# Performance work log

Measured on AMD Instinct MI355X. Metric: run time of the kernel, lower is better.

## Reference

```python
import jax, jax.numpy as jnp
import numpy as np

INP = 1024          # inp_size
N = 8000            # n_neurons
NE = 6400           # n_e_neurons = 0.8*N
NI = 1600           # n_i_neurons = 0.2*N
TS = 1000           # ts_sim = t_sim/dt = 1.0/0.001
PRB0, PRB1 = 200, 1000  # probe window in timesteps
DT = 0.001
TAU = 0.02
VTH = 0.5
RATE = 0.5          # rate_scale
NORM = float(PRB1 - PRB0)  # spike_p_norm


def setup_inputs() -> dict:
    key = jax.random.key(0)
    k1, k2, k3, k4, k5, k6 = jax.random.split(key, 6)
    inp = jax.random.uniform(k1, (INP,), dtype=jnp.float32)
    A = INP + N
    # Sparse random recurrent weights, faithful in structure to init_w:
    # rows [0:INP+NE] carry excitatory (positive) weights, last NI rows inhibitory (negative).
    sign = jnp.concatenate([jnp.ones(INP + NE, jnp.float32), -jnp.ones(NI, jnp.float32)])[:, None]
    mask_e = (jax.random.uniform(k2, (A, NE)) < 0.05).astype(jnp.float32)
    w_ae = sign * mask_e * jax.random.uniform(k3, (A, NE), dtype=jnp.float32) * 0.1
    mask_i = (jax.random.uniform(k4, (A, NI)) < 0.05).astype(jnp.float32)
    w_ai = sign * mask_i * jax.random.uniform(k5, (A, NI), dtype=jnp.float32) * 0.1
    # Precomputed per-timestep uniform noise (replaces torch.rand_like in the loop)
    rand_p = jax.random.uniform(k6, (TS, INP), dtype=jnp.float32)
    return {"inp": inp, "w_ae": w_ae, "w_ai": w_ai, "rand_p": rand_p}


def reference(inp, w_ae, w_ai, rand_p):
    inp_s = inp * RATE
    decay = 1.0 - DT / TAU  # vmem += -vmem/tau*dt  ==  vmem *= (1 - dt/tau)

    def step(carry, r):
        vmem, sl, slp = carry  # spike_l, spike_l_prev as float32 {0,1}
        sp = (r <= inp_s).astype(jnp.float32)  # Poisson input spikes
        v = vmem * decay
        # excitatory targets see prev-step E spikes + current I spikes; inhibitory the reverse
        in_e = jnp.concatenate([sp, slp[:NE], sl[NE:]])   # [INP+N]
        in_i = jnp.concatenate([sp, sl[:NE], slp[NE:]])   # [INP+N]
        v = v + jnp.concatenate([in_e @ w_ae, in_i @ w_ai])  # [N]
        new_sl = (v >= VTH).astype(jnp.float32)
        v = v * (1.0 - new_sl)  # reset fired neurons to 0
        return (v, new_sl, sl), new_sl[:NE]

    init = (jnp.zeros(N, jnp.float32), jnp.zeros(N, jnp.float32), jnp.zeros(N, jnp.float32))
    _, e_spikes = jax.lax.scan(step, init, rand_p)  # [TS, NE]
    sumspike_e = e_spikes[PRB0:PRB1].sum(axis=0)
    return sumspike_e / NORM
```

## Files before the change

### kernel.cpp

```cpp
#include <hip/hip_runtime.h>
#include <stdint.h>

#define INP_N   1024
#define NE_N    6400
#define NI_N    1600
#define NCOL    8000
#define TS_N    1000
#define PRB0_T  200
#define TSPLIT  16
#define NCHUNK  12
#define CAPTOT  992
#define IN_ENT  112
#define BC      64
#define CAPQ    36
#define CAPMAX  88

enum : size_t {
  ROWS_OFF = 0,
  VALS_OFF = ROWS_OFF + (size_t)CAPTOT * NCOL * 2,
  CNT_OFF  = VALS_OFF + (size_t)CAPTOT * NCOL * 4,
  CSUM_OFF = CNT_OFF  + (size_t)NCHUNK * NCOL * 4,
  INPM_OFF = CSUM_OFF + (size_t)NCHUNK * NCOL * 4,
  DRV_OFF  = INPM_OFF + (size_t)TS_N * 16 * 8,
  SE_OFF   = DRV_OFF  + (size_t)TS_N * NCOL * 4,
  SI_OFF   = SE_OFF   + (size_t)NCOL * 4,
  FLG_OFF  = SI_OFF   + (size_t)NCOL * 4,
  STV_OFF  = FLG_OFF  + (size_t)TS_N * 4,
  STR_OFF  = STV_OFF  + (size_t)8192 * 4,
  STT_OFF  = STR_OFF  + (size_t)512 * 8,
  SAB_OFF  = STT_OFF  + (size_t)8 * 4,
  AFL_OFF  = SAB_OFF  + 4,
  MNP_OFF  = AFL_OFF  + 4,
  MNW_OFF  = MNP_OFF  + 32 * 4,
  OVF_OFF  = MNW_OFF  + 64 * 4,
  STG_OFF  = OVF_OFF  + 4,
};

__device__ __forceinline__ void chunk_info(int c, int& j0, int& len, int& cap, int& off) {
  if (c < 2) { j0 = c * 512;            len = 512; cap = 56; off = c * 56; }
  else       { j0 = 1024 + (c - 2) * 800; len = 800; cap = 88; off = 112 + (c - 2) * 88; }
}

__global__ void k_spikes(const float* __restrict__ rand_p,
                         const float* __restrict__ inp,
                         unsigned long long* __restrict__ inpmask,
                         float* __restrict__ gv, unsigned long long* __restrict__ gring,
                         int* __restrict__ gtot, int* __restrict__ ovf) {
  int gid = blockIdx.x * blockDim.x + threadIdx.x;
  if (gid < 8192) gv[gid] = 0.f;
  if (gid < 512)  gring[gid] = 0ull;
  if (gid < 8)    gtot[gid] = 0;
  if (gid == 0)   ovf[0] = 0;
  int i = gid & (INP_N - 1);
  int pred = rand_p[gid] <= inp[i] * 0.5f;
  unsigned long long b = __ballot(pred != 0);
  if ((threadIdx.x & 63) == 0) inpmask[gid >> 6] = b;
}

__global__ void __launch_bounds__(256) k_build(
    const float* __restrict__ w_ae, const float* __restrict__ w_ai,
    uint16_t* __restrict__ rows, float* __restrict__ vals,
    int* __restrict__ cnt, float* __restrict__ csum, int* __restrict__ ovf) {
  __shared__ uint16_t rs_s[4 * CAPQ * BC];
  __shared__ float    vs_s[4 * CAPQ * BC];
  __shared__ int      kqs[4][BC];
  __shared__ float    sqs[4][BC];
  const int tid   = threadIdx.x;
  const int lane  = tid & 63;
  const int wv    = tid >> 6;
  const int chunk = blockIdx.y;
  const int col0  = blockIdx.x * BC;
  int j0, len, cap, off;
  chunk_info(chunk, j0, len, cap, off);
  const float* W; int nc, cc0;
  if (col0 < NE_N) { W = w_ae; nc = NE_N; cc0 = col0; }
  else             { W = w_ai; nc = NI_N; cc0 = col0 - NE_N; }

  const int qlen = len >> 2;
  const int j0w  = j0 + wv * qlen;
  const float* Wc = W + (size_t)j0w * nc + cc0 + lane;

  float cur[16], nxt[16];
  #pragma unroll
  for (int r = 0; r < 16; ++r)
    cur[r] = Wc[(size_t)r * nc];

  int k = 0; float s = 0.f; int ovfl = 0;
  for (int t0 = 0; t0 < qlen; t0 += 16) {
    const int nt = t0 + 16;
    if (nt < qlen) {
      #pragma unroll
      for (int r = 0; r < 16; ++r) {
        int rq = nt + r; rq = rq < qlen ? rq : qlen - 1;
        nxt[r] = Wc[(size_t)rq * nc];
      }
    }
    const int rlim = (qlen - t0) < 16 ? (qlen - t0) : 16;
    #pragma unroll
    for (int r = 0; r < 16; ++r) {
      if (r < rlim) {
        float w = cur[r];
        if (w != 0.f) {
          if (k < CAPQ) {
            rs_s[(wv * CAPQ + k) * BC + lane] = (uint16_t)(j0w + t0 + r);
            vs_s[(wv * CAPQ + k) * BC + lane] = w;
            s += w; ++k;
          } else ovfl = 1;
        }
      }
    }
    #pragma unroll
    for (int r = 0; r < 16; ++r) cur[r] = nxt[r];
  }
  kqs[wv][lane] = k;
  sqs[wv][lane] = s;
  if (ovfl) atomicOr(ovf, 1);
  __syncthreads();

  const int col = lane;
  const int k0 = kqs[0][col], k1 = kqs[1][col], k2 = kqs[2][col], k3 = kqs[3][col];
  const int c1 = k0, c2 = k0 + k1, c3 = c2 + k2, ktot = c3 + k3;
  if (tid < BC) {
    cnt[chunk * NCOL + col0 + col]  = ktot < cap ? ktot : cap;
    csum[chunk * NCOL + col0 + col] = ((sqs[0][col] + sqs[1][col]) + sqs[2][col]) + sqs[3][col];
    if (ktot > cap) atomicOr(ovf, 1);
  }
  const size_t gb = (size_t)off * NCOL + col0;
  for (int kk = wv; kk < cap; kk += 4) {
    uint16_t rr = (uint16_t)j0; float vv = 0.f;
    if (kk < ktot) {
      int q, loc;
      if      (kk < c1) { q = 0; loc = kk; }
      else if (kk < c2) { q = 1; loc = kk - c1; }
      else if (kk < c3) { q = 2; loc = kk - c2; }
      else              { q = 3; loc = kk - c3; }
      rr = rs_s[(q * CAPQ + loc) * BC + col];
      vv = vs_s[(q * CAPQ + loc) * BC + col];
    }
    rows[gb + (size_t)kk * NCOL + col] = rr;
    vals[gb + (size_t)kk * NCOL + col] = vv;
  }
}

__global__ void __launch_bounds__(256) k_proof(
    const float* __restrict__ csum, float* __restrict__ sE, float* __restrict__ sI,
    const float* __restrict__ vals, float* __restrict__ minpart, float* __restrict__ mwpart) {
  const int tid = threadIdx.x;
  const int b = blockIdx.x;
  float m = 1e30f;
  if (b < 32) {
    int col = b * 256 + tid;
    if (col < NCOL) {
      float se = 0.f;
      #pragma unroll
      for (int c = 2; c <= 9; ++c) se += csum[c * NCOL + col];
      float si = csum[10 * NCOL + col] + csum[11 * NCOL + col];
      sE[col] = se;
      sI[col] = si;
      m = se + si;
    }
  } else {
    const int n = IN_ENT * NCOL;
    for (int i = (b - 32) * 256 + tid; i < n; i += 64 * 256)
      m = fminf(m, vals[i]);
  }
  #pragma unroll
  for (int o = 32; o; o >>= 1) m = fminf(m, __shfl_down(m, o));
  __shared__ float w4[4];
  if ((tid & 63) == 0) w4[tid >> 6] = m;
  __syncthreads();
  if (tid == 0) {
    float r = fminf(fminf(w4[0], w4[1]), fminf(w4[2], w4[3]));
    if (b < 32) minpart[b] = r; else mwpart[b - 32] = r;
  }
}

__global__ void k_strong(const float* __restrict__ minpart, const float* __restrict__ mwpart,
                         const int* __restrict__ ovf, int* __restrict__ strongp) {
  int t = threadIdx.x;
  float mb = (t < 32) ? minpart[t] : 1e30f;
  float mw = mwpart[t];
  #pragma unroll
  for (int o = 32; o; o >>= 1) {
    mb = fminf(mb, __shfl_down(mb, o));
    mw = fminf(mw, __shfl_down(mw, o));
  }
  if (t == 0)
    strongp[0] = (mb >= 1.0f && mw >= 0.0f && ovf[0] == 0) ? 1 : 0;
}

__global__ void __launch_bounds__(256) k_drive(
    const uint16_t* __restrict__ rows, const float* __restrict__ vals,
    const unsigned long long* __restrict__ inpmask, float* __restrict__ drive,
    const int* __restrict__ strongp, const int* __restrict__ sabp, int pass) {
  int t0, t1;
  if (pass == 0) {
    if (strongp[0]) {
      if (blockIdx.y >= 4) return;
      t0 = blockIdx.y * 4; t1 = t0 + 4;
    } else { t0 = blockIdx.y * 40; t1 = t0 + 40; }
  } else {
    if (!strongp[0] || sabp[0]) return;
    t0 = blockIdx.y * 40; t1 = t0 + 40;
    if (blockIdx.y == 0) t0 = TSPLIT;
  }
  __shared__ uint16_t rs[IN_ENT * 64];
  __shared__ float    vs[IN_ENT * 64];
  __shared__ float    act0[INP_N];
  __shared__ float    psum[4][64];
  const int tid = threadIdx.x, lane = tid & 63, ph = tid >> 6;
  const int col0 = blockIdx.x * 64;
  for (int idx = tid; idx < IN_ENT * 64; idx += 256) {
    int k = idx >> 6, l = idx & 63;
    rs[idx] = rows[(size_t)k * NCOL + col0 + l];
    vs[idx] = vals[(size_t)k * NCOL + col0 + l];
  }
  __syncthreads();
  for (int t = t0; t < t1; ++t) {
    #pragma unroll
    for (int i = tid; i < INP_N; i += 256)
      act0[i] = (float)((inpmask[(size_t)t * 16 + (i >> 6)] >> (i & 63)) & 1ull);
    __syncthreads();
    float acc = 0.f;
    for (int k = ph; k < IN_ENT; k += 4)
      acc += vs[k * 64 + lane] * act0[rs[k * 64 + lane]];
    psum[ph][lane] = acc;
    __syncthreads();
    if (ph == 0)
      drive[(size_t)t * NCOL + col0 + lane] =
        ((psum[0][lane] + psum[1][lane]) + psum[2][lane]) + psum[3][lane];
    __syncthreads();
  }
}

__global__ void __launch_bounds__(512) k_step(
    const uint16_t* __restrict__ rows, const float* __restrict__ vals,
    const int* __restrict__ cnt, const float* __restrict__ sE,
    const float* __restrict__ sI, const float* __restrict__ drive,
    float* __restrict__ gv, unsigned long long* __restrict__ gring,
    int* __restrict__ gtot, const int* __restrict__ strongp, int t) {
  __shared__ unsigned long long m[128];
  __shared__ float psum[8][64];
  const int tid = threadIdx.x, lane = tid & 63, ph = tid >> 6;
  const int blk = blockIdx.x;
  const bool isE = (blk < 100);
  const int sw = t & 3, s1 = (t + 3) & 3, s2 = (t + 2) & 3;

  const bool full1 = (gtot[s1] == NE_N) && (gtot[4 + s1] == NI_N);
  const bool full2 = (gtot[s2] == NE_N) && (gtot[4 + s2] == NI_N);
  if (strongp[0] && full1 && full2) {
    if (tid == 0) {
      gring[sw * 128 + blk] = ~0ull;
      if (blk == 0) { gtot[sw] = NE_N; gtot[4 + sw] = NI_N; }
    }
    return;
  }

  const int sEs = isE ? s2 : s1;
  const int sIs = isE ? s1 : s2;
  const int col = blk * 64 + lane;

  if (tid < 100)      m[tid] = gring[sEs * 128 + tid];
  else if (tid < 125) m[tid] = gring[sIs * 128 + tid];
  const int pEv = gtot[sEs];
  const int pIv = gtot[4 + sIs];
  if (blk == 0 && tid == 0) { gtot[(t + 1) & 3] = 0; gtot[4 + ((t + 1) & 3)] = 0; }
  __syncthreads();

  float acc = 0.f;
  if (pEv > 0 && pEv < NE_N) {
    for (int c = 2; c <= 9; ++c) {
      int cn = cnt[c * NCOL + col];
      size_t base = (size_t)(112 + (c - 2) * 88) * NCOL + col;
      for (int k = ph; k < cn; k += 8) {
        int r = rows[base + (size_t)k * NCOL] - 1024;
        float wv = vals[base + (size_t)k * NCOL];
        if ((m[r >> 6] >> (r & 63)) & 1ull) acc += wv;
      }
    }
  }
  if (pIv > 0 && pIv < NI_N) {
    for (int c = 10; c <= 11; ++c) {
      int cn = cnt[c * NCOL + col];
      size_t base = (size_t)(112 + (c - 2) * 88) * NCOL + col;
      for (int k = ph; k < cn; k += 8) {
        int r = rows[base + (size_t)k * NCOL] - 1024;
        float wv = vals[base + (size_t)k * NCOL];
        if ((m[r >> 6] >> (r & 63)) & 1ull) acc += wv;
      }
    }
  }
  psum[ph][lane] = acc;
  __syncthreads();

  if (ph == 0) {
    float tot = drive[(size_t)t * NCOL + col]
              + ((psum[0][lane] + psum[1][lane]) + (psum[2][lane] + psum[3][lane]))
              + ((psum[4][lane] + psum[5][lane]) + (psum[6][lane] + psum[7][lane]));
    if (pEv == NE_N) tot += sE[col];
    if (pIv == NI_N) tot += sI[col];
    float vn = gv[col] * 0.95f + tot;
    int s = (vn >= 0.5f) ? 1 : 0;
    gv[col] = s ? 0.f : vn;
    unsigned long long bal = __ballot(s);
    int pc = __popcll(bal);
    if (lane == 0) {
      gring[sw * 128 + blk] = bal;
      if (isE) atomicAdd(&gtot[sw], pc);
      else     atomicAdd(&gtot[4 + sw], pc);
    }
  }
}

__global__ void k_sab(const int* __restrict__ gtot, int* __restrict__ sab) {
  sab[0] = (gtot[1] == NE_N && gtot[2] == NE_N && gtot[3] == NE_N &&
            gtot[5] == NI_N && gtot[6] == NI_N && gtot[7] == NI_N) ? 1 : 0;
}

__global__ void __launch_bounds__(256) k_check2(
    const float* __restrict__ drive, const float* __restrict__ sE,
    const float* __restrict__ sI, int* __restrict__ flag,
    const int* __restrict__ strongp, const int* __restrict__ sabp) {
  if (strongp[0] && sabp[0]) return;
  const int t = blockIdx.x, tid = threadIdx.x;
  const float* dr = drive + (size_t)t * NCOL;
  int nb = 0;
  for (int col = tid; col < NCOL; col += 256) {
    float vn = (dr[col] + sE[col]) + sI[col];
    nb += (vn >= 0.5f) ? 0 : 1;
  }
  #pragma unroll
  for (int o = 32; o; o >>= 1) nb += __shfl_down(nb, o);
  __shared__ int w4[4];
  if ((tid & 63) == 0) w4[tid >> 6] = nb;
  __syncthreads();
  if (tid == 0) flag[t] = ((w4[0] + w4[1]) + (w4[2] + w4[3])) == 0 ? 1 : 0;
}

__global__ void k_fin(const int* __restrict__ flag, const int* __restrict__ strongp,
                      int* __restrict__ allflag) {
  const int tid = threadIdx.x;
  if (strongp[0]) { if (tid == 0) allflag[0] = 1; return; }
  int bad = 0;
  for (int i = TSPLIT + tid; i < TS_N; i += 256) bad += (flag[i] == 0) ? 1 : 0;
  #pragma unroll
  for (int o = 32; o; o >>= 1) bad += __shfl_down(bad, o);
  __shared__ int w4[4];
  if ((tid & 63) == 0) w4[tid >> 6] = bad;
  __syncthreads();
  if (tid == 0) allflag[0] = ((w4[0] + w4[1]) + (w4[2] + w4[3])) == 0 ? 1 : 0;
}

__global__ void __launch_bounds__(1024) k_simB(
    const uint16_t* __restrict__ rows, const float* __restrict__ vals,
    const int* __restrict__ cnt, const float* __restrict__ sE,
    const float* __restrict__ sI, const float* __restrict__ drive,
    const int* __restrict__ flag,
    const float* __restrict__ stv, const unsigned long long* __restrict__ str_,
    const int* __restrict__ stt, const int* __restrict__ sab,
    const int* __restrict__ allflag, float* __restrict__ out) {
  __shared__ unsigned long long ring[4][128];
  __shared__ int pEtot[4], pItot[4];
  __shared__ int flagsL[TS_N];
  __shared__ int fastexit;

  const int tid  = threadIdx.x;
  const int lane = tid & 63;
  const int wv   = tid >> 6;

  if (tid == 0) fastexit = (sab[0] != 0) && (allflag[0] != 0);
  __syncthreads();

  if (fastexit) {
    #pragma unroll
    for (int p = 0; p < 8; ++p) {
      int col = p * 1024 + tid;
      if (col < NE_N) out[col] = 1.0f;
    }
    return;
  }

  for (int i = tid; i < 512; i += 1024) (&ring[0][0])[i] = str_[i];
  if (tid < 4) { pEtot[tid] = stt[tid]; pItot[tid] = stt[4 + tid]; }
  for (int i = tid; i < TS_N; i += 1024) flagsL[i] = flag[i];

  float v[8], sEr[8], sIr[8];
  int spk[8];
  #pragma unroll
  for (int p = 0; p < 8; ++p) {
    int col = p * 1024 + tid;
    sEr[p] = (col < NCOL) ? sE[col] : 0.f;
    sIr[p] = (col < NCOL) ? sI[col] : 0.f;
    v[p] = (col < NCOL) ? stv[col] : 0.f; spk[p] = 0;
  }
  int spkAll = 0, fastAge = 0;
  __syncthreads();

  for (int t = TSPLIT; t < TS_N; ++t) {
    const int sw = t & 3, s1 = (t + 3) & 3, s2 = (t + 2) & 3;
    int pE1, pI1, pE2, pI2;
    if (fastAge >= 2)      { pE1 = pE2 = NE_N; pI1 = pI2 = NI_N; }
    else if (fastAge == 1) { pE1 = NE_N; pI1 = NI_N; pE2 = pEtot[s2]; pI2 = pItot[s2]; }
    else                   { pE1 = pEtot[s1]; pI1 = pItot[s1]; pE2 = pEtot[s2]; pI2 = pItot[s2]; }
    const bool satE1 = (pE1 == NE_N), satE2 = (pE2 == NE_N);
    const bool satI1 = (pI1 == NI_N), satI2 = (pI2 == NI_N);

    if (satE1 && satI1 && satE2 && satI2 && flagsL[t]) {
      if (t >= PRB0_T) ++spkAll;
      ++fastAge;
      continue;
    }

    if (fastAge > 0) {
      for (int i = tid; i < 128; i += 1024) {
        ring[s1][i] = ~0ull;
        if (fastAge >= 2) ring[s2][i] = ~0ull;
      }
    }
    if (tid == 0) {
      if (fastAge > 0) {
        pEtot[s1] = NE_N; pItot[s1] = NI_N;
        if (fastAge >= 2) { pEtot[s2] = NE_N; pItot[s2] = NI_N; }
      }
      pEtot[sw] = 0; pItot[sw] = 0;
    }
    __syncthreads();
    fastAge = 0;

    const float* dr = drive + (size_t)t * NCOL;
    int myE = 0, myI = 0;
    #pragma unroll
    for (int p = 0; p < 8; ++p) {
      int col = p * 1024 + tid;
      bool isEcol = col < NE_N;
      int pEv = isEcol ? pE2 : pE1;
      int pIv = isEcol ? pI1 : pI2;
      int sEs = isEcol ? s2 : s1;
      int sIs = isEcol ? s1 : s2;
      float tot = (col < NCOL) ? dr[col] : 0.f;
      if (col < NCOL) {
        if (pEv == NE_N) tot += sEr[p];
        else if (pEv > 0) {
          for (int c = 2; c <= 9; ++c) {
            int cn = cnt[c * NCOL + col];
            size_t base = (size_t)(112 + (c - 2) * 88) * NCOL + col;
            for (int k = 0; k < cn; ++k) {
              int j = rows[base + (size_t)k * NCOL];
              float wval = vals[base + (size_t)k * NCOL];
              int r = j - 1024;
              if ((ring[sEs][r >> 6] >> (r & 63)) & 1ull) tot += wval;
            }
          }
        }
        if (pIv == NI_N) tot += sIr[p];
        else if (pIv > 0) {
          for (int c = 10; c <= 11; ++c) {
            int cn = cnt[c * NCOL + col];
            size_t base = (size_t)(112 + (c - 2) * 88) * NCOL + col;
            for (int k = 0; k < cn; ++k) {
              int j = rows[base + (size_t)k * NCOL];
              float wval = vals[base + (size_t)k * NCOL];
              int r = j - 1024;
              if ((ring[sIs][r >> 6] >> (r & 63)) & 1ull) tot += wval;
            }
          }
        }
      }
      float vn = v[p] * 0.95f + tot;
      int s = (col < NCOL) && (vn >= 0.5f);
      v[p] = s ? 0.f : vn;
      if (t >= PRB0_T && isEcol) spk[p] += s;
      unsigned long long bal = __ballot(s);
      int word = p * 16 + wv;
      if (word < 125) {
        int pc = __popcll(bal);
        if (word < 100) myE += pc; else myI += pc;
        if (lane == 0) ring[sw][word] = bal;
      }
    }
    if (lane == 0) { atomicAdd(&pEtot[sw], myE); atomicAdd(&pItot[sw], myI); }
    __syncthreads();
  }

  #pragma unroll
  for (int p = 0; p < 8; ++p) {
    int col = p * 1024 + tid;
    if (col < NE_N) out[col] = (float)(spk[p] + spkAll) / 800.0f;
  }
}

extern "C" void kernel_launch(void* const* d_in, const int* in_sizes, int n_in,
                              void* d_out, int out_size, void* d_ws, size_t ws_size,
                              hipStream_t stream) {
  const float* inp    = (const float*)d_in[0];
  const float* w_ae   = (const float*)d_in[1];
  const float* w_ai   = (const float*)d_in[2];
  const float* rand_p = (const float*)d_in[3];

  char* ws = (char*)d_ws;
  uint16_t*           rows    = (uint16_t*)(ws + ROWS_OFF);
  float*              vals    = (float*)(ws + VALS_OFF);
  int*                cnt     = (int*)(ws + CNT_OFF);
  float*              csum    = (float*)(ws + CSUM_OFF);
  unsigned long long* inpmask = (unsigned long long*)(ws + INPM_OFF);
  float*              drive   = (float*)(ws + DRV_OFF);
  float*              sEa     = (float*)(ws + SE_OFF);
  float*              sIa     = (float*)(ws + SI_OFF);
  int*                flag    = (int*)(ws + FLG_OFF);
  float*              gv      = (float*)(ws + STV_OFF);
  unsigned long long* gring   = (unsigned long long*)(ws + STR_OFF);
  int*                gtot    = (int*)(ws + STT_OFF);
  int*                sab     = (int*)(ws + SAB_OFF);
  int*                afl     = (int*)(ws + AFL_OFF);
  float*              minpart = (float*)(ws + MNP_OFF);
  float*              mwpart  = (float*)(ws + MNW_OFF);
  int*                ovf     = (int*)(ws + OVF_OFF);
  int*                strg    = (int*)(ws + STG_OFF);

  k_spikes<<<(TS_N * INP_N) / 256, 256, 0, stream>>>(rand_p, inp, inpmask, gv, gring, gtot, ovf);
  k_build<<<dim3(NCOL / BC, NCHUNK), 256, 0, stream>>>(w_ae, w_ai, rows, vals, cnt, csum, ovf);
  k_proof<<<96, 256, 0, stream>>>(csum, sEa, sIa, vals, minpart, mwpart);
  k_strong<<<1, 64, 0, stream>>>(minpart, mwpart, ovf, strg);
  k_drive<<<dim3(125, 25), 256, 0, stream>>>(rows, vals, inpmask, drive, strg, sab, 0);
  for (int t = 0; t < TSPLIT; ++t)
    k_step<<<125, 512, 0, stream>>>(rows, vals, cnt, sEa, sIa, drive, gv, gring, gtot, strg, t);
  k_sab<<<1, 1, 0, stream>>>(gtot, sab);
  k_drive<<<dim3(125, 25), 256, 0, stream>>>(rows, vals, inpmask, drive, strg, sab, 1);
  k_check2<<<TS_N, 256, 0, stream>>>(drive, sEa, sIa, flag, strg, sab);
  k_fin<<<1, 256, 0, stream>>>(flag, strg, afl);
  k_simB<<<1, 1024, 0, stream>>>(rows, vals, cnt, sEa, sIa, drive, flag,
                                 gv, gring, gtot, sab, afl, (float*)d_out);
}
```

Measured before the change: 587.4 us.

## Merge launches: fold spike/strong kernels, fuse last steps into grid-synced tail kernel

Removes the k_spikes and k_strong launches. State zeroing moves into k_build, the strong-condition reduction runs in the last-arriving k_proof block through an atomic counter, and k_drive computes Poisson input spikes inline from rand_p. The last six of the sixteen per-step k_step launches are replaced by one persistent k_tail kernel that synchronises its blocks with a spin barrier. k_build skips padding writes for recurrent chunks, and k_check2 uses 125 looping blocks. The aim is less launch overhead and fewer global atomics, at the cost of a software grid barrier that relies on all 125 blocks being resident at once.

```diff
diff --git a/kernel.cpp b/kernel.cpp
--- a/kernel.cpp
+++ b/kernel.cpp
@@ -13,15 +13,14 @@
 #define IN_ENT  112
 #define BC      64
 #define CAPQ    36
-#define CAPMAX  88
+#define NBLD    (125 * 12)
 
 enum : size_t {
   ROWS_OFF = 0,
   VALS_OFF = ROWS_OFF + (size_t)CAPTOT * NCOL * 2,
   CNT_OFF  = VALS_OFF + (size_t)CAPTOT * NCOL * 4,
   CSUM_OFF = CNT_OFF  + (size_t)NCHUNK * NCOL * 4,
-  INPM_OFF = CSUM_OFF + (size_t)NCHUNK * NCOL * 4,
-  DRV_OFF  = INPM_OFF + (size_t)TS_N * 16 * 8,
+  DRV_OFF  = CSUM_OFF + (size_t)NCHUNK * NCOL * 4,
   SE_OFF   = DRV_OFF  + (size_t)TS_N * NCOL * 4,
   SI_OFF   = SE_OFF   + (size_t)NCOL * 4,
   FLG_OFF  = SI_OFF   + (size_t)NCOL * 4,
@@ -32,8 +31,9 @@
   AFL_OFF  = SAB_OFF  + 4,
   MNP_OFF  = AFL_OFF  + 4,
   MNW_OFF  = MNP_OFF  + 32 * 4,
-  OVF_OFF  = MNW_OFF  + 64 * 4,
-  STG_OFF  = OVF_OFF  + 4,
+  STG_OFF  = MNW_OFF  + 64 * 4,
+  OVA_OFF  = STG_OFF  + 4,
+  CTR_OFF  = OVA_OFF  + (size_t)NBLD * 4,
 };
 
 __device__ __forceinline__ void chunk_info(int c, int& j0, int& len, int& cap, int& off) {
@@ -41,35 +41,30 @@
   else       { j0 = 1024 + (c - 2) * 800; len = 800; cap = 88; off = 112 + (c - 2) * 88; }
 }
 
-__global__ void k_spikes(const float* __restrict__ rand_p,
-                         const float* __restrict__ inp,
-                         unsigned long long* __restrict__ inpmask,
-                         float* __restrict__ gv, unsigned long long* __restrict__ gring,
-                         int* __restrict__ gtot, int* __restrict__ ovf) {
-  int gid = blockIdx.x * blockDim.x + threadIdx.x;
-  if (gid < 8192) gv[gid] = 0.f;
-  if (gid < 512)  gring[gid] = 0ull;
-  if (gid < 8)    gtot[gid] = 0;
-  if (gid == 0)   ovf[0] = 0;
-  int i = gid & (INP_N - 1);
-  int pred = rand_p[gid] <= inp[i] * 0.5f;
-  unsigned long long b = __ballot(pred != 0);
-  if ((threadIdx.x & 63) == 0) inpmask[gid >> 6] = b;
-}
-
 __global__ void __launch_bounds__(256) k_build(
     const float* __restrict__ w_ae, const float* __restrict__ w_ai,
     uint16_t* __restrict__ rows, float* __restrict__ vals,
-    int* __restrict__ cnt, float* __restrict__ csum, int* __restrict__ ovf) {
+    int* __restrict__ cnt, float* __restrict__ csum, int* __restrict__ ovfA,
+    float* __restrict__ gv, unsigned long long* __restrict__ gring,
+    int* __restrict__ gtot, unsigned int* __restrict__ ctr) {
   __shared__ uint16_t rs_s[4 * CAPQ * BC];
   __shared__ float    vs_s[4 * CAPQ * BC];
   __shared__ int      kqs[4][BC];
   __shared__ float    sqs[4][BC];
+  __shared__ int      wovf[4];
   const int tid   = threadIdx.x;
   const int lane  = tid & 63;
   const int wv    = tid >> 6;
   const int chunk = blockIdx.y;
   const int col0  = blockIdx.x * BC;
+
+  if (blockIdx.x == 0 && blockIdx.y == 0) {
+    for (int i = tid; i < 8192; i += 256) gv[i] = 0.f;
+    for (int i = tid; i < 512; i += 256)  gring[i] = 0ull;
+    if (tid < 8) gtot[tid] = 0;
+    if (tid < 2) ctr[tid] = 0u;
+  }
+
   int j0, len, cap, off;
   chunk_info(chunk, j0, len, cap, off);
   const float* W; int nc, cc0;
@@ -82,8 +77,7 @@
 
   float cur[16], nxt[16];
   #pragma unroll
-  for (int r = 0; r < 16; ++r)
-    cur[r] = Wc[(size_t)r * nc];
+  for (int r = 0; r < 16; ++r) cur[r] = Wc[(size_t)r * nc];
 
   int k = 0; float s = 0.f; int ovfl = 0;
   for (int t0 = 0; t0 < qlen; t0 += 16) {
@@ -114,7 +108,9 @@
   }
   kqs[wv][lane] = k;
   sqs[wv][lane] = s;
-  if (ovfl) atomicOr(ovf, 1);
+  if (lane == 0) wovf[wv] = 0;
+  int anyo = __any(ovfl);
+  if (lane == 0) wovf[wv] = anyo;
   __syncthreads();
 
   const int col = lane;
@@ -123,10 +119,14 @@
   if (tid < BC) {
     cnt[chunk * NCOL + col0 + col]  = ktot < cap ? ktot : cap;
     csum[chunk * NCOL + col0 + col] = ((sqs[0][col] + sqs[1][col]) + sqs[2][col]) + sqs[3][col];
-    if (ktot > cap) atomicOr(ovf, 1);
-  }
+    unsigned long long capov = __ballot(ktot > cap);
+    if (tid == 0)
+      ovfA[blockIdx.y * gridDim.x + blockIdx.x] =
+        (capov ? 1 : 0) | wovf[0] | wovf[1] | wovf[2] | wovf[3];
+  }
+  const int wlim = (chunk < 2) ? cap : (ktot < cap ? ktot : cap);
   const size_t gb = (size_t)off * NCOL + col0;
-  for (int kk = wv; kk < cap; kk += 4) {
+  for (int kk = wv; kk < wlim; kk += 4) {
     uint16_t rr = (uint16_t)j0; float vv = 0.f;
     if (kk < ktot) {
       int q, loc;
@@ -144,9 +144,12 @@
 
 __global__ void __launch_bounds__(256) k_proof(
     const float* __restrict__ csum, float* __restrict__ sE, float* __restrict__ sI,
-    const float* __restrict__ vals, float* __restrict__ minpart, float* __restrict__ mwpart) {
+    const float* __restrict__ vals, float* __restrict__ minpart, float* __restrict__ mwpart,
+    const int* __restrict__ ovfA, unsigned int* __restrict__ ctr, int* __restrict__ strongp) {
   const int tid = threadIdx.x;
   const int b = blockIdx.x;
+  __shared__ float w4[4];
+  __shared__ int lastS;
   float m = 1e30f;
   if (b < 32) {
     int col = b * 256 + tid;
@@ -166,32 +169,44 @@
   }
   #pragma unroll
   for (int o = 32; o; o >>= 1) m = fminf(m, __shfl_down(m, o));
-  __shared__ float w4[4];
   if ((tid & 63) == 0) w4[tid >> 6] = m;
   __syncthreads();
   if (tid == 0) {
     float r = fminf(fminf(w4[0], w4[1]), fminf(w4[2], w4[3]));
     if (b < 32) minpart[b] = r; else mwpart[b - 32] = r;
-  }
-}
-
-__global__ void k_strong(const float* __restrict__ minpart, const float* __restrict__ mwpart,
-                         const int* __restrict__ ovf, int* __restrict__ strongp) {
-  int t = threadIdx.x;
-  float mb = (t < 32) ? minpart[t] : 1e30f;
-  float mw = mwpart[t];
+    __threadfence();
+    unsigned p = __hip_atomic_fetch_add(&ctr[0], 1u, __ATOMIC_ACQ_REL, __HIP_MEMORY_SCOPE_AGENT);
+    lastS = (p == 95) ? 1 : 0;
+  }
+  __syncthreads();
+  if (!lastS) return;
+  __threadfence();
+  float mb = (tid < 32) ? __hip_atomic_load(&minpart[tid], __ATOMIC_RELAXED, __HIP_MEMORY_SCOPE_AGENT) : 1e30f;
+  float mw = (tid < 64) ? __hip_atomic_load(&mwpart[tid],  __ATOMIC_RELAXED, __HIP_MEMORY_SCOPE_AGENT) : 1e30f;
+  int ov = 0;
+  for (int i = tid; i < NBLD; i += 256)
+    ov |= __hip_atomic_load(&ovfA[i], __ATOMIC_RELAXED, __HIP_MEMORY_SCOPE_AGENT);
   #pragma unroll
   for (int o = 32; o; o >>= 1) {
     mb = fminf(mb, __shfl_down(mb, o));
     mw = fminf(mw, __shfl_down(mw, o));
-  }
-  if (t == 0)
-    strongp[0] = (mb >= 1.0f && mw >= 0.0f && ovf[0] == 0) ? 1 : 0;
+    ov |= __shfl_down(ov, o);
+  }
+  __shared__ float fm[4], fw[4]; __shared__ int fo[4];
+  if ((tid & 63) == 0) { fm[tid >> 6] = mb; fw[tid >> 6] = mw; fo[tid >> 6] = ov; }
+  __syncthreads();
+  if (tid == 0) {
+    float MB = fminf(fminf(fm[0], fm[1]), fminf(fm[2], fm[3]));
+    float MW = fminf(fminf(fw[0], fw[1]), fminf(fw[2], fw[3]));
+    int   OV = fo[0] | fo[1] | fo[2] | fo[3];
+    strongp[0] = (MB >= 1.0f && MW >= 0.0f && OV == 0) ? 1 : 0;
+  }
 }
 
 __global__ void __launch_bounds__(256) k_drive(
     const uint16_t* __restrict__ rows, const float* __restrict__ vals,
-    const unsigned long long* __restrict__ inpmask, float* __restrict__ drive,
+    const float* __restrict__ rand_p, const float* __restrict__ inp,
+    float* __restrict__ drive,
     const int* __restrict__ strongp, const int* __restrict__ sabp, int pass) {
   int t0, t1;
   if (pass == 0) {
@@ -206,6 +221,7 @@
   }
   __shared__ uint16_t rs[IN_ENT * 64];
   __shared__ float    vs[IN_ENT * 64];
+  __shared__ float    inps[INP_N];
   __shared__ float    act0[INP_N];
   __shared__ float    psum[4][64];
   const int tid = threadIdx.x, lane = tid & 63, ph = tid >> 6;
@@ -215,11 +231,12 @@
     rs[idx] = rows[(size_t)k * NCOL + col0 + l];
     vs[idx] = vals[(size_t)k * NCOL + col0 + l];
   }
+  for (int i = tid; i < INP_N; i += 256) inps[i] = inp[i] * 0.5f;
   __syncthreads();
   for (int t = t0; t < t1; ++t) {
     #pragma unroll
     for (int i = tid; i < INP_N; i += 256)
-      act0[i] = (float)((inpmask[(size_t)t * 16 + (i >> 6)] >> (i & 63)) & 1ull);
+      act0[i] = (rand_p[(size_t)t * INP_N + i] <= inps[i]) ? 1.f : 0.f;
     __syncthreads();
     float acc = 0.f;
     for (int k = ph; k < IN_ENT; k += 4)
@@ -312,6 +329,100 @@
   }
 }
 
+__global__ void __launch_bounds__(512) k_tail(
+    const uint16_t* __restrict__ rows, const float* __restrict__ vals,
+    const int* __restrict__ cnt, const float* __restrict__ sE,
+    const float* __restrict__ sI, const float* __restrict__ drive,
+    float* __restrict__ gv, unsigned long long* __restrict__ gring,
+    int* __restrict__ gtot, const int* __restrict__ strongp,
+    unsigned int* __restrict__ ctr) {
+  __shared__ unsigned long long m[128];
+  __shared__ float psum[8][64];
+  const int tid = threadIdx.x, lane = tid & 63, ph = tid >> 6;
+  const int blk = blockIdx.x;
+  const bool isE = (blk < 100);
+
+  const bool full8 = (gtot[0] == NE_N) && (gtot[4] == NI_N);
+  const bool full9 = (gtot[1] == NE_N) && (gtot[5] == NI_N);
+  if (strongp[0] && full8 && full9) {
+    if (blk == 0) {
+      for (int i = tid; i < 512; i += 512) gring[i] = ~0ull;
+      if (tid < 4) { gtot[tid] = NE_N; gtot[4 + tid] = NI_N; }
+    }
+    return;
+  }
+
+  for (int t = 10; t < 16; ++t) {
+    const int sw = t & 3, s1 = (t + 3) & 3, s2 = (t + 2) & 3;
+    const int sEs = isE ? s2 : s1, sIs = isE ? s1 : s2;
+    if (tid < 100)
+      m[tid] = __hip_atomic_load(&gring[sEs * 128 + tid], __ATOMIC_RELAXED, __HIP_MEMORY_SCOPE_AGENT);
+    else if (tid < 125)
+      m[tid] = __hip_atomic_load(&gring[sIs * 128 + tid], __ATOMIC_RELAXED, __HIP_MEMORY_SCOPE_AGENT);
+    const int pEv = __hip_atomic_load(&gtot[sEs], __ATOMIC_RELAXED, __HIP_MEMORY_SCOPE_AGENT);
+    const int pIv = __hip_atomic_load(&gtot[4 + sIs], __ATOMIC_RELAXED, __HIP_MEMORY_SCOPE_AGENT);
+    if (blk == 0 && tid == 0) {
+      __hip_atomic_store(&gtot[(t + 1) & 3], 0, __ATOMIC_RELAXED, __HIP_MEMORY_SCOPE_AGENT);
+      __hip_atomic_store(&gtot[4 + ((t + 1) & 3)], 0, __ATOMIC_RELAXED, __HIP_MEMORY_SCOPE_AGENT);
+    }
+    __syncthreads();
+
+    const int col = blk * 64 + lane;
+    float acc = 0.f;
+    if (pEv > 0 && pEv < NE_N) {
+      for (int c = 2; c <= 9; ++c) {
+        int cn = cnt[c * NCOL + col];
+        size_t base = (size_t)(112 + (c - 2) * 88) * NCOL + col;
+        for (int k = ph; k < cn; k += 8) {
+          int r = rows[base + (size_t)k * NCOL] - 1024;
+          float wv = vals[base + (size_t)k * NCOL];
+          if ((m[r >> 6] >> (r & 63)) & 1ull) acc += wv;
+        }
+      }
+    }
+    if (pIv > 0 && pIv < NI_N) {
+      for (int c = 10; c <= 11; ++c) {
+        int cn = cnt[c * NCOL + col];
+        size_t base = (size_t)(112 + (c - 2) * 88) * NCOL + col;
+        for (int k = ph; k < cn; k += 8) {
+          int r = rows[base + (size_t)k * NCOL] - 1024;
+          float wv = vals[base + (size_t)k * NCOL];
+          if ((m[r >> 6] >> (r & 63)) & 1ull) acc += wv;
+        }
+      }
+    }
+    psum[ph][lane] = acc;
+    __syncthreads();
+
+    if (ph == 0) {
+      float tot = drive[(size_t)t * NCOL + col]
+                + ((psum[0][lane] + psum[1][lane]) + (psum[2][lane] + psum[3][lane]))
+                + ((psum[4][lane] + psum[5][lane]) + (psum[6][lane] + psum[7][lane]));
+      if (pEv == NE_N) tot += sE[col];
+      if (pIv == NI_N) tot += sI[col];
+      float vn = gv[col] * 0.95f + tot;
+      int s = (vn >= 0.5f) ? 1 : 0;
+      gv[col] = s ? 0.f : vn;
+      unsigned long long bal = __ballot(s);
+      int pc = __popcll(bal);
+      if (lane == 0) {
+        __hip_atomic_store(&gring[sw * 128 + blk], bal, __ATOMIC_RELAXED, __HIP_MEMORY_SCOPE_AGENT);
+        if (isE) atomicAdd(&gtot[sw], pc);
+        else     atomicAdd(&gtot[4 + sw], pc);
+      }
+    }
+    __syncthreads();
+    if (tid == 0) {
+      __threadfence();
+      __hip_atomic_fetch_add(&ctr[1], 1u, __ATOMIC_RELEASE, __HIP_MEMORY_SCOPE_AGENT);
+      const unsigned tgt = (unsigned)(t - 9) * 125;
+      while (__hip_atomic_load(&ctr[1], __ATOMIC_ACQUIRE, __HIP_MEMORY_SCOPE_AGENT) < tgt)
+        __builtin_amdgcn_s_sleep(1);
+    }
+    __syncthreads();
+  }
+}
+
 __global__ void k_sab(const int* __restrict__ gtot, int* __restrict__ sab) {
   sab[0] = (gtot[1] == NE_N && gtot[2] == NE_N && gtot[3] == NE_N &&
             gtot[5] == NI_N && gtot[6] == NI_N && gtot[7] == NI_N) ? 1 : 0;
@@ -322,19 +433,22 @@
     const float* __restrict__ sI, int* __restrict__ flag,
     const int* __restrict__ strongp, const int* __restrict__ sabp) {
   if (strongp[0] && sabp[0]) return;
-  const int t = blockIdx.x, tid = threadIdx.x;
-  const float* dr = drive + (size_t)t * NCOL;
-  int nb = 0;
-  for (int col = tid; col < NCOL; col += 256) {
-    float vn = (dr[col] + sE[col]) + sI[col];
-    nb += (vn >= 0.5f) ? 0 : 1;
-  }
-  #pragma unroll
-  for (int o = 32; o; o >>= 1) nb += __shfl_down(nb, o);
+  const int tid = threadIdx.x;
   __shared__ int w4[4];
-  if ((tid & 63) == 0) w4[tid >> 6] = nb;
-  __syncthreads();
-  if (tid == 0) flag[t] = ((w4[0] + w4[1]) + (w4[2] + w4[3])) == 0 ? 1 : 0;
+  for (int t = blockIdx.x; t < TS_N; t += 125) {
+    const float* dr = drive + (size_t)t * NCOL;
+    int nb = 0;
+    for (int col = tid; col < NCOL; col += 256) {
+      float vn = (dr[col] + sE[col]) + sI[col];
+      nb += (vn >= 0.5f) ? 0 : 1;
+    }
+    #pragma unroll
+    for (int o = 32; o; o >>= 1) nb += __shfl_down(nb, o);
+    if ((tid & 63) == 0) w4[tid >> 6] = nb;
+    __syncthreads();
+    if (tid == 0) flag[t] = ((w4[0] + w4[1]) + (w4[2] + w4[3])) == 0 ? 1 : 0;
+    __syncthreads();
+  }
 }
 
 __global__ void k_fin(const int* __restrict__ flag, const int* __restrict__ strongp,
@@ -502,7 +616,6 @@
   float*              vals    = (float*)(ws + VALS_OFF);
   int*                cnt     = (int*)(ws + CNT_OFF);
   float*              csum    = (float*)(ws + CSUM_OFF);
-  unsigned long long* inpmask = (unsigned long long*)(ws + INPM_OFF);
   float*              drive   = (float*)(ws + DRV_OFF);
   float*              sEa     = (float*)(ws + SE_OFF);
   float*              sIa     = (float*)(ws + SI_OFF);
@@ -514,19 +627,20 @@
   int*                afl     = (int*)(ws + AFL_OFF);
   float*              minpart = (float*)(ws + MNP_OFF);
   float*              mwpart  = (float*)(ws + MNW_OFF);
-  int*                ovf     = (int*)(ws + OVF_OFF);
   int*                strg    = (int*)(ws + STG_OFF);
-
-  k_spikes<<<(TS_N * INP_N) / 256, 256, 0, stream>>>(rand_p, inp, inpmask, gv, gring, gtot, ovf);
-  k_build<<<dim3(NCOL / BC, NCHUNK), 256, 0, stream>>>(w_ae, w_ai, rows, vals, cnt, csum, ovf);
-  k_proof<<<96, 256, 0, stream>>>(csum, sEa, sIa, vals, minpart, mwpart);
-  k_strong<<<1, 64, 0, stream>>>(minpart, mwpart, ovf, strg);
-  k_drive<<<dim3(125, 25), 256, 0, stream>>>(rows, vals, inpmask, drive, strg, sab, 0);
-  for (int t = 0; t < TSPLIT; ++t)
+  int*                ovfA    = (int*)(ws + OVA_OFF);
+  unsigned int*       ctr     = (unsigned int*)(ws + CTR_OFF);
+
+  k_build<<<dim3(NCOL / BC, NCHUNK), 256, 0, stream>>>(w_ae, w_ai, rows, vals, cnt, csum,
+                                                       ovfA, gv, gring, gtot, ctr);
+  k_proof<<<96, 256, 0, stream>>>(csum, sEa, sIa, vals, minpart, mwpart, ovfA, ctr, strg);
+  k_drive<<<dim3(125, 25), 256, 0, stream>>>(rows, vals, rand_p, inp, drive, strg, sab, 0);
+  for (int t = 0; t < 10; ++t)
     k_step<<<125, 512, 0, stream>>>(rows, vals, cnt, sEa, sIa, drive, gv, gring, gtot, strg, t);
+  k_tail<<<125, 512, 0, stream>>>(rows, vals, cnt, sEa, sIa, drive, gv, gring, gtot, strg, ctr);
   k_sab<<<1, 1, 0, stream>>>(gtot, sab);
-  k_drive<<<dim3(125, 25), 256, 0, stream>>>(rows, vals, inpmask, drive, strg, sab, 1);
-  k_check2<<<TS_N, 256, 0, stream>>>(drive, sEa, sIa, flag, strg, sab);
+  k_drive<<<dim3(125, 25), 256, 0, stream>>>(rows, vals, rand_p, inp, drive, strg, sab, 1);
+  k_check2<<<125, 256, 0, stream>>>(drive, sEa, sIa, flag, strg, sab);
   k_fin<<<1, 256, 0, stream>>>(flag, strg, afl);
   k_simB<<<1, 1024, 0, stream>>>(rows, vals, cnt, sEa, sIa, drive, flag,
                                  gv, gring, gtot, sab, afl, (float*)d_out);
```

New measurement: 589.9 us. Within noise of the previous version (+0.4%).
